# Kernel optimization log

Hardware: AMD Instinct MI355X
Metric: run time of the kernel (lower is better)

## Reference

```python
import jax, jax.numpy as jnp
import numpy as np

C_IN = 12      # total channels (rgb-noised + hidden)
C_NOISE = 3    # noise-prediction channels
HID = 128      # rule-MLP hidden size
PERC = 48      # perception channels (depthwise, 48/12 = 4 filters per channel)
TDIM = 256     # sinusoidal time-embedding dim


def setup_inputs() -> dict:
    key = jax.random.key(0)
    ks = jax.random.split(key, 12)
    B, H, W = 16, 256, 256
    x = jax.random.normal(ks[0], (B, C_NOISE, H, W), jnp.float32)
    hidden_channels = jax.random.normal(ks[1], (B, C_IN - C_NOISE, H, W), jnp.float32)
    t = jax.random.randint(ks[2], (B,), 0, 1000)
    # depthwise 3x3 perceive conv: torch weight shape [out=48, in/groups=1, 3, 3]
    w_perceive = jax.random.normal(ks[3], (PERC, 1, 3, 3), jnp.float32) * 0.1
    b_perceive = jax.random.normal(ks[4], (PERC,), jnp.float32) * 0.01
    # 1x1 convs of the rule network, stored as [out, in]
    w1 = jax.random.normal(ks[5], (HID, PERC), jnp.float32) * 0.1
    b1 = jax.random.normal(ks[6], (HID,), jnp.float32) * 0.01
    w2 = jax.random.normal(ks[7], (HID, HID), jnp.float32) * 0.05
    b2 = jax.random.normal(ks[8], (HID,), jnp.float32) * 0.01
    # conv3 is zero-initialized in the original; random here for test coverage
    w3 = jax.random.normal(ks[9], (C_IN, HID), jnp.float32) * 0.05
    # time embedding Linear(256 -> c_noise)
    w_time = jax.random.normal(ks[10], (C_NOISE, TDIM), jnp.float32) * 0.1
    b_time = jax.random.normal(ks[11], (C_NOISE,), jnp.float32) * 0.01
    return dict(x=x, hidden_channels=hidden_channels, t=t,
                w_perceive=w_perceive, b_perceive=b_perceive,
                w1=w1, b1=b1, w2=w2, b2=b2, w3=w3,
                w_time=w_time, b_time=b_time)


def _pos_encoding(t, channels):
    # t: [B] int -> [B, channels] sinusoidal embedding (torch repeat-then-scale layout)
    inv_freq = 1.0 / (10000.0 ** (jnp.arange(0, channels, 2, dtype=jnp.float32) / channels))
    ang = t.astype(jnp.float32)[:, None] * inv_freq  # [B, channels//2]
    return jnp.concatenate([jnp.sin(ang), jnp.cos(ang)], axis=-1)


def reference(x, hidden_channels, t, w_perceive, b_perceive, w1, b1, w2, b2, w3, w_time, b_time):
    # concat noised channels with hidden state channels -> [B, 12, H, W]
    xf = jnp.concatenate([x, hidden_channels], axis=1)
    # depthwise 3x3 conv, 'same' padding, groups = C_IN
    perc = jax.lax.conv_general_dilated(
        xf, w_perceive, window_strides=(1, 1), padding='SAME',
        feature_group_count=C_IN,
        dimension_numbers=('NCHW', 'OIHW', 'NCHW')) + b_perceive[None, :, None, None]
    # rule network: three 1x1 convs (pointwise MLP) with ReLUs
    h = jax.nn.relu(jnp.einsum('bchw,oc->bohw', perc, w1) + b1[None, :, None, None])
    h = jax.nn.relu(jnp.einsum('bchw,oc->bohw', h, w2) + b2[None, :, None, None])
    out = jnp.einsum('bchw,oc->bohw', h, w3)  # no bias
    # time embedding: sinusoidal -> SiLU -> Linear -> broadcast over H, W
    pe = _pos_encoding(t, TDIM)                       # [B, 256]
    emb = jax.nn.silu(pe) @ w_time.T + b_time         # [B, 3]
    noise_prediction = out[:, :C_NOISE] + emb[:, :, None, None]
    hidden_out = out[:, C_NOISE:]
    return (hidden_out, noise_prediction)
```

## Files before the change

### kernel.cpp

```cpp
#include <hip/hip_runtime.h>


#define ACT_S 128
#define PERC_S 64
#define NOISE_BASE 9437184

#define WSF_OFF 13312
#define WSF_BP 0
#define WSF_B1 48
#define WSF_B2 176
#define WSF_WP 304
#define WSF_EMB 736

typedef short bf16x8 __attribute__((ext_vector_type(8)));
typedef float f32x4 __attribute__((ext_vector_type(4)));

__device__ __forceinline__ short f2bf(float f) {
    union { float f; unsigned u; } cv; cv.f = f;
    unsigned r = cv.u + 0x7FFFu + ((cv.u >> 16) & 1u);
    return (short)(r >> 16);
}
__device__ __forceinline__ unsigned pk2bf(float f0, float f1) {
    union { float f; unsigned u; } a, b; a.f = f0; b.f = f1;
    return __builtin_amdgcn_perm(b.u + 0x8000u, a.u + 0x8000u, 0x07060302u);
}

__global__ void prep_emb_kernel(const float* __restrict__ wpg, const float* __restrict__ bpg,
                                const float* __restrict__ w1g, const float* __restrict__ b1g,
                                const float* __restrict__ w2g, const float* __restrict__ b2g,
                                const float* __restrict__ w3g,
                                const int* __restrict__ t,
                                const float* __restrict__ wt, const float* __restrict__ bt,
                                short* __restrict__ wsb, float* __restrict__ wsf)
{
    if (blockIdx.x < 107) {
        int i = blockIdx.x * 256 + threadIdx.x;
        if (i < 8192) {
            int o = i >> 6, c = i & 63;
            wsb[i] = (c < 48) ? f2bf(w1g[o * 48 + c]) : (short)0;
        } else if (i < 24576) {
            wsb[i] = f2bf(w2g[i - 8192]);
        } else if (i < 26624) {
            int k = i - 24576;
            wsb[i] = (k < 1536) ? f2bf(w3g[k]) : (short)0;
        } else if (i < 26672) {
            wsf[WSF_BP + (i - 26624)] = bpg[i - 26624];
        } else if (i < 26800) {
            wsf[WSF_B1 + (i - 26672)] = b1g[i - 26672];
        } else if (i < 26928) {
            wsf[WSF_B2 + (i - 26800)] = b2g[i - 26800];
        } else if (i < 27360) {
            wsf[WSF_WP + (i - 26928)] = wpg[i - 26928];
        }
        return;
    }
    int b = blockIdx.x - 107;
    int lane = threadIdx.x;
    if (lane >= 64) return;
    float tv = (float)t[b];
    float s0 = 0.f, s1 = 0.f, s2 = 0.f;
    const float LOG1E4 = 9.210340371976184f;
    #pragma unroll
    for (int ii = 0; ii < 2; ++ii) {
        int i = lane + ii * 64;
        float invf = __expf(-LOG1E4 * (float)i * (1.0f / 128.0f));
        float ang = tv * invf;
        float sn = sinf(ang), cs = cosf(ang);
        float ss = sn / (1.0f + __expf(-sn));
        float sc = cs / (1.0f + __expf(-cs));
        s0 += ss * wt[0 * 256 + i] + sc * wt[0 * 256 + i + 128];
        s1 += ss * wt[1 * 256 + i] + sc * wt[1 * 256 + i + 128];
        s2 += ss * wt[2 * 256 + i] + sc * wt[2 * 256 + i + 128];
    }
    #pragma unroll
    for (int off = 32; off; off >>= 1) {
        s0 += __shfl_down(s0, off);
        s1 += __shfl_down(s1, off);
        s2 += __shfl_down(s2, off);
    }
    if (lane == 0) {
        wsf[WSF_EMB + b * 3 + 0] = s0 + bt[0];
        wsf[WSF_EMB + b * 3 + 1] = s1 + bt[1];
        wsf[WSF_EMB + b * 3 + 2] = s2 + bt[2];
    }
}

__global__ __launch_bounds__(256, 3) void canet_main(
    const float* __restrict__ xg,
    const float* __restrict__ hg,
    const short* __restrict__ wsb,
    const float* __restrict__ wsf,
    float* __restrict__ outg)
{
    __shared__ __align__(16) short percS[64 * PERC_S];
    __shared__ __align__(16) short h1S[64 * ACT_S];
    __shared__ __align__(16) short h2S[64 * ACT_S];
    __shared__ __align__(16) float wp_s[592];
    __shared__ float bp_s[48];

    const int tid = threadIdx.x;
    const int b = blockIdx.x >> 8;
    const int y = blockIdx.x & 255;

    for (int i = tid; i < 576; i += 256) {
        int oc = i / 12, k = i % 12;
        wp_s[i + (oc / 12) * 4] = (k < 9) ? wsf[WSF_WP + oc * 9 + k] : 0.0f;
    }
    if (tid < 48) bp_s[tid] = wsf[WSF_BP + tid];

    {
        int r = tid >> 2, c = tid & 3;
        *(uint2*)(percS + r * PERC_S + ((48 + c * 4) ^ ((r & 7) << 3))) = uint2{0u, 0u};
    }

    const int wv = tid >> 6;
    const int lane = tid & 63;
    const int m = lane & 15;
    const int q = lane >> 4;
    const int rsw = (m & 7) << 3;

    bf16x8 w1f[2][2], w2f[2][4], w3f[4];
    #pragma unroll
    for (int j = 0; j < 2; ++j) {
        int n = wv * 32 + j * 16 + m;
        #pragma unroll
        for (int ks = 0; ks < 2; ++ks)
            w1f[j][ks] = *(const bf16x8*)(wsb + n * 64 + ks * 32 + q * 8);
        #pragma unroll
        for (int ks = 0; ks < 4; ++ks)
            w2f[j][ks] = *(const bf16x8*)(wsb + 8192 + n * 128 + ks * 32 + q * 8);
    }
    #pragma unroll
    for (int ks = 0; ks < 4; ++ks)
        w3f[ks] = *(const bf16x8*)(wsb + 24576 + m * 128 + ks * 32 + q * 8);

    f32x4 b1v[2], b2v[2];
    #pragma unroll
    for (int j = 0; j < 2; ++j) {
        b1v[j] = *(const f32x4*)(wsf + WSF_B1 + wv * 32 + j * 16 + q * 4);
        b2v[j] = *(const f32x4*)(wsf + WSF_B2 + wv * 32 + j * 16 + q * 4);
    }
    const float embv = (m < 3) ? wsf[WSF_EMB + b * 3 + m] : 0.0f;

    const float* src3[3];
    #pragma unroll
    for (int i3 = 0; i3 < 3; ++i3) {
        int ic = 3 * q + i3;
        src3[i3] = (ic < 3) ? (xg + (((size_t)b * 3 + ic) << 16))
                            : (hg + (((size_t)b * 9 + (ic - 3)) << 16));
    }

    __syncthreads();

    for (int it = 0; it < 4; ++it) {
        const int x0 = it * 64;
        const int px = x0 + wv * 16 + m;

        {
            const int xm1 = px - (px > 0);
            const int xp1 = px + (px < 255);
            const bool okl = (px > 0), okr = (px < 255);
            short* prow = percS + (wv * 16 + m) * PERC_S;
            const bool interior = (y >= 1) && (y <= 254);
            #pragma unroll
            for (int i3 = 0; i3 < 3; ++i3) {
                const float* s = src3[i3];
                float tap[9];
                if (interior) {
                    #pragma unroll
                    for (int ky = 0; ky < 3; ++ky) {
                        const float* rp = s + (y + ky - 1) * 256;
                        float c0 = rp[xm1], c1 = rp[px], c2 = rp[xp1];
                        tap[ky * 3 + 0] = okl ? c0 : 0.0f;
                        tap[ky * 3 + 1] = c1;
                        tap[ky * 3 + 2] = okr ? c2 : 0.0f;
                    }
                } else {
                    #pragma unroll
                    for (int ky = 0; ky < 3; ++ky) {
                        int yy = y + ky - 1;
                        bool yok = (yy >= 0) && (yy < 256);
                        const float* rp = s + (yok ? yy : y) * 256;
                        float c0 = rp[xm1], c1 = rp[px], c2 = rp[xp1];
                        tap[ky * 3 + 0] = (yok && okl) ? c0 : 0.0f;
                        tap[ky * 3 + 1] = yok ? c1 : 0.0f;
                        tap[ky * 3 + 2] = (yok && okr) ? c2 : 0.0f;
                    }
                }
                float v[4];
                #pragma unroll
                for (int r = 0; r < 4; ++r) {
                    int oc = 12 * q + 4 * i3 + r;
                    const float* wrow = &wp_s[oc * 12 + 4 * q];
                    f32x4 w0 = *(const f32x4*)wrow;
                    f32x4 w1_ = *(const f32x4*)(wrow + 4);
                    float a = bp_s[oc];
                    a += w0[0] * tap[0] + w0[1] * tap[1] + w0[2] * tap[2] + w0[3] * tap[3];
                    a += w1_[0] * tap[4] + w1_[1] * tap[5] + w1_[2] * tap[6] + w1_[3] * tap[7];
                    a += wrow[8] * tap[8];
                    v[r] = a;
                }
                uint2 pk;
                pk.x = pk2bf(v[0], v[1]);
                pk.y = pk2bf(v[2], v[3]);
                *(uint2*)(prow + ((12 * q + 4 * i3) ^ rsw)) = pk;
            }
        }
        __syncthreads();

        #pragma unroll
        for (int nt = 0; nt < 4; ++nt) {
            f32x4 c0 = b1v[0], c1 = b1v[1];
            #pragma unroll
            for (int ks = 0; ks < 2; ++ks) {
                bf16x8 p = *(const bf16x8*)(percS + (nt * 16 + m) * PERC_S + ((ks * 32 + q * 8) ^ rsw));
                c0 = __builtin_amdgcn_mfma_f32_16x16x32_bf16(w1f[0][ks], p, c0, 0, 0, 0);
                c1 = __builtin_amdgcn_mfma_f32_16x16x32_bf16(w1f[1][ks], p, c1, 0, 0, 0);
            }
            short* drow = h1S + (nt * 16 + m) * ACT_S;
            uint2 pk;
            pk.x = pk2bf(fmaxf(c0[0], 0.f), fmaxf(c0[1], 0.f));
            pk.y = pk2bf(fmaxf(c0[2], 0.f), fmaxf(c0[3], 0.f));
            *(uint2*)(drow + ((wv * 32 + q * 4) ^ rsw)) = pk;
            pk.x = pk2bf(fmaxf(c1[0], 0.f), fmaxf(c1[1], 0.f));
            pk.y = pk2bf(fmaxf(c1[2], 0.f), fmaxf(c1[3], 0.f));
            *(uint2*)(drow + ((wv * 32 + q * 4 + 16) ^ rsw)) = pk;
        }
        __syncthreads();

        #pragma unroll
        for (int nt = 0; nt < 4; ++nt) {
            f32x4 c0 = b2v[0], c1 = b2v[1];
            #pragma unroll
            for (int ks = 0; ks < 4; ++ks) {
                bf16x8 a = *(const bf16x8*)(h1S + (nt * 16 + m) * ACT_S + ((ks * 32 + q * 8) ^ rsw));
                c0 = __builtin_amdgcn_mfma_f32_16x16x32_bf16(w2f[0][ks], a, c0, 0, 0, 0);
                c1 = __builtin_amdgcn_mfma_f32_16x16x32_bf16(w2f[1][ks], a, c1, 0, 0, 0);
            }
            short* drow = h2S + (nt * 16 + m) * ACT_S;
            uint2 pk;
            pk.x = pk2bf(fmaxf(c0[0], 0.f), fmaxf(c0[1], 0.f));
            pk.y = pk2bf(fmaxf(c0[2], 0.f), fmaxf(c0[3], 0.f));
            *(uint2*)(drow + ((wv * 32 + q * 4) ^ rsw)) = pk;
            pk.x = pk2bf(fmaxf(c1[0], 0.f), fmaxf(c1[1], 0.f));
            pk.y = pk2bf(fmaxf(c1[2], 0.f), fmaxf(c1[3], 0.f));
            *(uint2*)(drow + ((wv * 32 + q * 4 + 16) ^ rsw)) = pk;
        }
        __syncthreads();

        {
            f32x4 acc = {0.f, 0.f, 0.f, 0.f};
            #pragma unroll
            for (int ks = 0; ks < 4; ++ks) {
                bf16x8 a = *(const bf16x8*)(h2S + (wv * 16 + m) * ACT_S + ((ks * 32 + q * 8) ^ rsw));
                acc = __builtin_amdgcn_mfma_f32_16x16x32_bf16(a, w3f[ks], acc, 0, 0, 0);
            }
            if (m < 12) {
                int xx0 = x0 + wv * 16 + q * 4;
                size_t idx;
                if (m < 3) {
                    idx = (size_t)NOISE_BASE + (((size_t)b * 3 + m) << 16) + (size_t)y * 256 + xx0;
                } else {
                    idx = (((size_t)b * 9 + (m - 3)) << 16) + (size_t)y * 256 + xx0;
                }
                f32x4 vst = {acc[0] + embv, acc[1] + embv, acc[2] + embv, acc[3] + embv};
                *(f32x4*)(outg + idx) = vst;
            }
        }
    }
}

extern "C" void kernel_launch(void* const* d_in, const int* in_sizes, int n_in,
                              void* d_out, int out_size, void* d_ws, size_t ws_size,
                              hipStream_t stream) {
    const float* xg  = (const float*)d_in[0];
    const float* hg  = (const float*)d_in[1];
    const int*   tg  = (const int*)  d_in[2];
    const float* wpg = (const float*)d_in[3];
    const float* bpg = (const float*)d_in[4];
    const float* w1g = (const float*)d_in[5];
    const float* b1g = (const float*)d_in[6];
    const float* w2g = (const float*)d_in[7];
    const float* b2g = (const float*)d_in[8];
    const float* w3g = (const float*)d_in[9];
    const float* wtg = (const float*)d_in[10];
    const float* btg = (const float*)d_in[11];
    float* outg = (float*)d_out;
    short* wsb  = (short*)d_ws;
    float* wsf  = (float*)d_ws + WSF_OFF;

    prep_emb_kernel<<<123, 256, 0, stream>>>(wpg, bpg, w1g, b1g, w2g, b2g, w3g,
                                             tg, wtg, btg, wsb, wsf);
    canet_main<<<4096, 256, 0, stream>>>(xg, hg, wsb, wsf, outg);
}
```

Measured before the change: 235.9 us.

## Prefetch next tile's conv taps, alias LDS buffers, raise occupancy to 4 blocks

Loads the 27 depthwise-conv input taps for the next 64-pixel tile into registers while the current tile's conv arithmetic and MLP run, hiding global load latency. The perception buffer and the second hidden buffer now share one LDS array, and the 3x3 weights are transposed so each tap reads four output channels with one vector load. Launch bounds go from 3 to 4 blocks per SM. An extra barrier at the end of each iteration guards the aliased buffer. The costs are higher register pressure from the 27-float prefetch under the tighter occupancy target, and one more synchronisation per iteration.

New measurement: 430.5 us. 1.82x slower.

```diff
diff --git a/kernel.cpp b/kernel.cpp
--- a/kernel.cpp
+++ b/kernel.cpp
@@ -2,7 +2,6 @@
 
 
 #define ACT_S 128
-#define PERC_S 64
 #define NOISE_BASE 9437184
 
 #define WSF_OFF 13312
@@ -50,7 +49,9 @@
         } else if (i < 26928) {
             wsf[WSF_B2 + (i - 26800)] = b2g[i - 26800];
         } else if (i < 27360) {
-            wsf[WSF_WP + (i - 26928)] = wpg[i - 26928];
+            int idx = i - 26928;
+            int oc = idx / 9, k = idx % 9;
+            wsf[WSF_WP + k * 48 + oc] = wpg[idx];
         }
         return;
     }
@@ -85,33 +86,24 @@
     }
 }
 
-__global__ __launch_bounds__(256, 3) void canet_main(
+__global__ __launch_bounds__(256, 4) void canet_main(
     const float* __restrict__ xg,
     const float* __restrict__ hg,
     const short* __restrict__ wsb,
     const float* __restrict__ wsf,
     float* __restrict__ outg)
 {
-    __shared__ __align__(16) short percS[64 * PERC_S];
+    __shared__ __align__(16) short bufA[64 * ACT_S];
     __shared__ __align__(16) short h1S[64 * ACT_S];
-    __shared__ __align__(16) short h2S[64 * ACT_S];
-    __shared__ __align__(16) float wp_s[592];
+    __shared__ __align__(16) float wpT_s[9 * 48];
     __shared__ float bp_s[48];
 
     const int tid = threadIdx.x;
     const int b = blockIdx.x >> 8;
     const int y = blockIdx.x & 255;
 
-    for (int i = tid; i < 576; i += 256) {
-        int oc = i / 12, k = i % 12;
-        wp_s[i + (oc / 12) * 4] = (k < 9) ? wsf[WSF_WP + oc * 9 + k] : 0.0f;
-    }
+    for (int i = tid; i < 432; i += 256) wpT_s[i] = wsf[WSF_WP + i];
     if (tid < 48) bp_s[tid] = wsf[WSF_BP + tid];
-
-    {
-        int r = tid >> 2, c = tid & 3;
-        *(uint2*)(percS + r * PERC_S + ((48 + c * 4) ^ ((r & 7) << 3))) = uint2{0u, 0u};
-    }
 
     const int wv = tid >> 6;
     const int lane = tid & 63;
@@ -149,6 +141,31 @@
         src3[i3] = (ic < 3) ? (xg + (((size_t)b * 3 + ic) << 16))
                             : (hg + (((size_t)b * 9 + (ic - 3)) << 16));
     }
+    int yoff[3]; bool yokk[3];
+    #pragma unroll
+    for (int ky = 0; ky < 3; ++ky) {
+        int yy = y + ky - 1;
+        yokk[ky] = (yy >= 0) && (yy < 256);
+        yoff[ky] = (yokk[ky] ? yy : y) * 256;
+    }
+
+    auto load_taps = [&](float (&tp)[27], int pxl) {
+        const int xm1 = pxl - (pxl > 0);
+        const int xp1 = pxl + (pxl < 255);
+        #pragma unroll
+        for (int i3 = 0; i3 < 3; ++i3) {
+            #pragma unroll
+            for (int ky = 0; ky < 3; ++ky) {
+                const float* rp = src3[i3] + yoff[ky];
+                tp[i3 * 9 + ky * 3 + 0] = rp[xm1];
+                tp[i3 * 9 + ky * 3 + 1] = rp[pxl];
+                tp[i3 * 9 + ky * 3 + 2] = rp[xp1];
+            }
+        }
+    };
+
+    float tp[27];
+    load_taps(tp, wv * 16 + m);
 
     __syncthreads();
 
@@ -157,54 +174,37 @@
         const int px = x0 + wv * 16 + m;
 
         {
-            const int xm1 = px - (px > 0);
-            const int xp1 = px + (px < 255);
             const bool okl = (px > 0), okr = (px < 255);
-            short* prow = percS + (wv * 16 + m) * PERC_S;
-            const bool interior = (y >= 1) && (y <= 254);
+            float tm[27];
             #pragma unroll
             for (int i3 = 0; i3 < 3; ++i3) {
-                const float* s = src3[i3];
-                float tap[9];
-                if (interior) {
-                    #pragma unroll
-                    for (int ky = 0; ky < 3; ++ky) {
-                        const float* rp = s + (y + ky - 1) * 256;
-                        float c0 = rp[xm1], c1 = rp[px], c2 = rp[xp1];
-                        tap[ky * 3 + 0] = okl ? c0 : 0.0f;
-                        tap[ky * 3 + 1] = c1;
-                        tap[ky * 3 + 2] = okr ? c2 : 0.0f;
-                    }
-                } else {
-                    #pragma unroll
-                    for (int ky = 0; ky < 3; ++ky) {
-                        int yy = y + ky - 1;
-                        bool yok = (yy >= 0) && (yy < 256);
-                        const float* rp = s + (yok ? yy : y) * 256;
-                        float c0 = rp[xm1], c1 = rp[px], c2 = rp[xp1];
-                        tap[ky * 3 + 0] = (yok && okl) ? c0 : 0.0f;
-                        tap[ky * 3 + 1] = yok ? c1 : 0.0f;
-                        tap[ky * 3 + 2] = (yok && okr) ? c2 : 0.0f;
-                    }
+                #pragma unroll
+                for (int ky = 0; ky < 3; ++ky) {
+                    int o = i3 * 9 + ky * 3;
+                    tm[o + 0] = (yokk[ky] && okl) ? tp[o + 0] : 0.0f;
+                    tm[o + 1] = yokk[ky] ? tp[o + 1] : 0.0f;
+                    tm[o + 2] = (yokk[ky] && okr) ? tp[o + 2] : 0.0f;
                 }
-                float v[4];
+            }
+            if (it < 3) load_taps(tp, px + 64);
+
+            short* prow = bufA + (wv * 16 + m) * ACT_S;
+            #pragma unroll
+            for (int i3 = 0; i3 < 3; ++i3) {
+                f32x4 acc = *(const f32x4*)(bp_s + 12 * q + 4 * i3);
                 #pragma unroll
-                for (int r = 0; r < 4; ++r) {
-                    int oc = 12 * q + 4 * i3 + r;
-                    const float* wrow = &wp_s[oc * 12 + 4 * q];
-                    f32x4 w0 = *(const f32x4*)wrow;
-                    f32x4 w1_ = *(const f32x4*)(wrow + 4);
-                    float a = bp_s[oc];
-                    a += w0[0] * tap[0] + w0[1] * tap[1] + w0[2] * tap[2] + w0[3] * tap[3];
-                    a += w1_[0] * tap[4] + w1_[1] * tap[5] + w1_[2] * tap[6] + w1_[3] * tap[7];
-                    a += wrow[8] * tap[8];
-                    v[r] = a;
+                for (int k = 0; k < 9; ++k) {
+                    f32x4 w4 = *(const f32x4*)(wpT_s + k * 48 + 12 * q + 4 * i3);
+                    float t = tm[i3 * 9 + k];
+                    acc[0] += w4[0] * t; acc[1] += w4[1] * t;
+                    acc[2] += w4[2] * t; acc[3] += w4[3] * t;
                 }
                 uint2 pk;
-                pk.x = pk2bf(v[0], v[1]);
-                pk.y = pk2bf(v[2], v[3]);
+                pk.x = pk2bf(acc[0], acc[1]);
+                pk.y = pk2bf(acc[2], acc[3]);
                 *(uint2*)(prow + ((12 * q + 4 * i3) ^ rsw)) = pk;
             }
+            *(uint2*)(prow + ((48 + 4 * q) ^ rsw)) = uint2{0u, 0u};
         }
         __syncthreads();
 
@@ -213,7 +213,7 @@
             f32x4 c0 = b1v[0], c1 = b1v[1];
             #pragma unroll
             for (int ks = 0; ks < 2; ++ks) {
-                bf16x8 p = *(const bf16x8*)(percS + (nt * 16 + m) * PERC_S + ((ks * 32 + q * 8) ^ rsw));
+                bf16x8 p = *(const bf16x8*)(bufA + (nt * 16 + m) * ACT_S + ((ks * 32 + q * 8) ^ rsw));
                 c0 = __builtin_amdgcn_mfma_f32_16x16x32_bf16(w1f[0][ks], p, c0, 0, 0, 0);
                 c1 = __builtin_amdgcn_mfma_f32_16x16x32_bf16(w1f[1][ks], p, c1, 0, 0, 0);
             }
@@ -237,7 +237,7 @@
                 c0 = __builtin_amdgcn_mfma_f32_16x16x32_bf16(w2f[0][ks], a, c0, 0, 0, 0);
                 c1 = __builtin_amdgcn_mfma_f32_16x16x32_bf16(w2f[1][ks], a, c1, 0, 0, 0);
             }
-            short* drow = h2S + (nt * 16 + m) * ACT_S;
+            short* drow = bufA + (nt * 16 + m) * ACT_S;
             uint2 pk;
             pk.x = pk2bf(fmaxf(c0[0], 0.f), fmaxf(c0[1], 0.f));
             pk.y = pk2bf(fmaxf(c0[2], 0.f), fmaxf(c0[3], 0.f));
@@ -252,7 +252,7 @@
             f32x4 acc = {0.f, 0.f, 0.f, 0.f};
             #pragma unroll
             for (int ks = 0; ks < 4; ++ks) {
-                bf16x8 a = *(const bf16x8*)(h2S + (wv * 16 + m) * ACT_S + ((ks * 32 + q * 8) ^ rsw));
+                bf16x8 a = *(const bf16x8*)(bufA + (wv * 16 + m) * ACT_S + ((ks * 32 + q * 8) ^ rsw));
                 acc = __builtin_amdgcn_mfma_f32_16x16x32_bf16(a, w3f[ks], acc, 0, 0, 0);
             }
             if (m < 12) {
@@ -267,6 +267,7 @@
                 *(f32x4*)(outg + idx) = vst;
             }
         }
+        __syncthreads();
     }
 }
 
```
